# Optimization experiments

Hardware: AMD Instinct MI355X
Metric: run time of the kernel (lower is better)

Reference implementation:

```python
import jax, jax.numpy as jnp
import numpy as np

EMBED = 64
N, T, F = 8, 64, 512

def setup_inputs() -> dict:
    key = jax.random.key(0)
    ks = jax.random.split(key, 8)
    shp = (N, T, F, EMBED)
    s = 1.0 / np.sqrt(EMBED)
    return {
        "value": jax.random.normal(ks[0], shp, jnp.float32),
        "key": jax.random.normal(ks[1], shp, jnp.float32),
        "query": jax.random.normal(ks[2], shp, jnp.float32),
        "Wv": jax.random.normal(ks[3], (EMBED, EMBED), jnp.float32) * s,
        "Wk": jax.random.normal(ks[4], (EMBED, EMBED), jnp.float32) * s,
        "Wq": jax.random.normal(ks[5], (EMBED, EMBED), jnp.float32) * s,
        "Wo": jax.random.normal(ks[6], (EMBED, EMBED), jnp.float32) * s,
        "bo": jax.random.normal(ks[7], (EMBED,), jnp.float32) * 0.01,
    }

def reference(value, key, query, Wv, Wk, Wq, Wo, bo):
    # nn.Linear applies y = x @ W.T (no bias for v/k/q)
    values = jnp.einsum('ntfe,de->ntfd', value, Wv)
    keys = jnp.einsum('ntfe,de->ntfd', key, Wk)
    queries = jnp.einsum('ntfe,de->ntfd', query, Wq)
    # contract over time t; attend over freq (q,k); embed e is a batch dim
    energy = jnp.einsum('ntqe,ntke->neqk', queries, keys)  # [N,e,Fq,Fk]
    scale = jnp.asarray(EMBED, energy.dtype) ** 0.5
    attention = jax.nn.softmax(energy / scale, axis=3)
    out = jnp.einsum('neqk,ntke->ntqe', attention, values)  # [N,T,Fq,e]
    out = jnp.einsum('ntqe,de->ntqd', out, Wo) + bo
    return out
```

## Files before the change

kernel.cpp:

```cpp
#include <hip/hip_runtime.h>
#include <hip/hip_bf16.h>

#define T_ 64
#define F_ 512
#define E_ 64
#define N_ 8
#define PROJ_ELEMS ((size_t)N_ * E_ * F_ * T_)
#define NSLAB ((size_t)E_ * F_ * T_)

typedef short bf16x8 __attribute__((ext_vector_type(8)));
typedef unsigned short u16x8 __attribute__((ext_vector_type(8)));
typedef unsigned short u16x4 __attribute__((ext_vector_type(4)));
typedef float f32x4 __attribute__((ext_vector_type(4)));

static __device__ __forceinline__ f32x4 mfma_bf16(bf16x8 a, bf16x8 b, f32x4 c) {
  return __builtin_amdgcn_mfma_f32_16x16x32_bf16(a, b, c, 0, 0, 0);
}

static __device__ __forceinline__ unsigned short f2bf(float x) {
  union { float f; unsigned u; } v; v.f = x;
  unsigned r = v.u + 0x7fffu + ((v.u >> 16) & 1u);
  return (unsigned short)(r >> 16);
}
static __device__ __forceinline__ float bf2f(unsigned short s) {
  union { unsigned u; float f; } v; v.u = ((unsigned)s) << 16;
  return v.f;
}

static __device__ __forceinline__ unsigned pack_bf16(float lo, float hi) {
#if __has_builtin(__builtin_amdgcn_cvt_pk_bf16_f32)
  typedef __bf16 bf16x2_t __attribute__((ext_vector_type(2)));
  union { bf16x2_t v; unsigned u; } c;
  c.v = __builtin_amdgcn_cvt_pk_bf16_f32(lo, hi);
  return c.u;
#else
  return ((unsigned)f2bf(lo)) | (((unsigned)f2bf(hi)) << 16);
#endif
}

static __device__ __forceinline__ bool detect_f32(const unsigned short* w) {
  bool m = false;
#pragma unroll
  for (int i = 0; i < 64; ++i) m |= ((unsigned)(w[i] & 0x7F80u) >= 0x4000u);
  return m;
}

static __device__ __forceinline__ bf16x8 cvt8(const float* p) {
  float4 x0 = *(const float4*)p;
  float4 x1 = *(const float4*)(p + 4);
  bf16x8 t;
  t[0] = (short)f2bf(x0.x); t[1] = (short)f2bf(x0.y);
  t[2] = (short)f2bf(x0.z); t[3] = (short)f2bf(x0.w);
  t[4] = (short)f2bf(x1.x); t[5] = (short)f2bf(x1.y);
  t[6] = (short)f2bf(x1.z); t[7] = (short)f2bf(x1.w);
  return t;
}

__global__ __launch_bounds__(256) void proj_kernel(
    const void* __restrict__ Xv0, const void* __restrict__ Xv1,
    const void* __restrict__ Xv2, const void* __restrict__ Wv0,
    const void* __restrict__ Wv1, const void* __restrict__ Wv2,
    unsigned short* __restrict__ o0, unsigned short* __restrict__ o1,
    unsigned short* __restrict__ o2, int n_base, int which) {
  __shared__ unsigned short chunk[4 * 64 * 76];
  const int p = (which < 0) ? (int)blockIdx.z : which;
  const void* Xv = (p == 0) ? Xv0 : ((p == 1) ? Xv1 : Xv2);
  const void* Wv = (p == 0) ? Wv0 : ((p == 1) ? Wv1 : Wv2);
  unsigned short* out = (p == 0) ? o0 : ((p == 1) ? o1 : o2);
  const int nb = blockIdx.y;
  const int na = nb + ((p == 2) ? n_base : 0);
  const int f0 = blockIdx.x * 4;
  const int tid = (int)threadIdx.x;
  const int lane = tid & 63, wv = tid >> 6;
  const int lr = lane & 15, quad = lane >> 4;
  const bool f32m = detect_f32((const unsigned short*)Wv);

  bf16x8 wf[4][2];
  if (!f32m) {
    const unsigned short* W = (const unsigned short*)Wv;
#pragma unroll
    for (int dt = 0; dt < 4; ++dt)
#pragma unroll
      for (int h = 0; h < 2; ++h)
        wf[dt][h] = *(const bf16x8*)(W + (dt * 16 + lr) * 64 + h * 32 + quad * 8);
  } else {
    const float* W = (const float*)Wv;
#pragma unroll
    for (int dt = 0; dt < 4; ++dt)
#pragma unroll
      for (int h = 0; h < 2; ++h)
        wf[dt][h] = cvt8(W + (dt * 16 + lr) * 64 + h * 32 + quad * 8);
  }

#pragma unroll
  for (int f = 0; f < 4; ++f) {
    const size_t xoff =
        ((size_t)((na * T_ + wv * 16 + lr) * F_ + f0 + f)) * E_ + quad * 8;
    bf16x8 a0, a1;
    if (!f32m) {
      const unsigned short* xp = (const unsigned short*)Xv + xoff;
      a0 = *(const bf16x8*)xp;
      a1 = *(const bf16x8*)(xp + 32);
    } else {
      const float* xp = (const float*)Xv + xoff;
      a0 = cvt8(xp);
      a1 = cvt8(xp + 32);
    }
#pragma unroll
    for (int dt = 0; dt < 4; ++dt) {
      f32x4 acc = {0.f, 0.f, 0.f, 0.f};
      acc = mfma_bf16(a0, wf[dt][0], acc);
      acc = mfma_bf16(a1, wf[dt][1], acc);
      u16x4 pk;
      pk[0] = f2bf(acc[0]); pk[1] = f2bf(acc[1]);
      pk[2] = f2bf(acc[2]); pk[3] = f2bf(acc[3]);
      *(u16x4*)&chunk[(f * 64 + dt * 16 + lr) * 76 + wv * 16 + quad * 4] = pk;
    }
  }
  __syncthreads();
#pragma unroll
  for (int it = 0; it < 8; ++it) {
    const int slot = it * 256 + tid;
    const int row = slot >> 3;
    const int part = slot & 7;
    const int d = row >> 2;
    const int f = row & 3;
    uint4 v2 = *(const uint4*)&chunk[(f * 64 + d) * 76 + part * 8];
    *(uint4*)(out + ((size_t)((nb * E_ + d) * F_ + f0 + f)) * T_ + part * 8) = v2;
  }
}

__global__ __launch_bounds__(512, 4) void attn_kernel(
    unsigned short* __restrict__ Vp,
    const unsigned short* __restrict__ Kp,
    const unsigned short* __restrict__ Qp, int n_base) {
  __shared__ unsigned short Vlds[T_ * 520];
  __shared__ unsigned short Plds[8 * 16 * 36];
  const int e = blockIdx.x, nb = blockIdx.y;
  const int na = nb + n_base;
  const size_t base = ((size_t)(na * E_ + e)) * (size_t)(F_ * T_);
  const unsigned short* Vb = Vp + base;
  const unsigned short* Kb = Kp + base;
  const unsigned short* Qb = Qp + ((size_t)(nb * E_ + e)) * (size_t)(F_ * T_);
  unsigned short* Ob = Vp + base;
  const int tid = (int)threadIdx.x;

#pragma unroll
  for (int it = 0; it < 8; ++it) {
    int slot = it * 512 + tid;
    int t = slot & 63, kg = slot >> 6;
    u16x8 tv;
#pragma unroll
    for (int j = 0; j < 8; ++j) tv[j] = Vb[(kg * 8 + j) * 64 + t];
    *(u16x8*)&Vlds[t * 520 + kg * 8] = tv;
  }
  __syncthreads();

  const int lane = tid & 63, wv = tid >> 6;
  const int lr = lane & 15, quad = lane >> 4;
  unsigned short* Pl = Plds + wv * (16 * 36);
  const float cexp = 0.18033688011112042f;

#pragma unroll
  for (int iter = 0; iter < 2; ++iter) {
    const int q0 = (wv + iter * 8) * 32;
    bf16x8 qf[2][2];
#pragma unroll
    for (int qt = 0; qt < 2; ++qt) {
      const unsigned short* qp = Qb + (q0 + qt * 16 + lr) * 64 + quad * 8;
      qf[qt][0] = *(const bf16x8*)qp;
      qf[qt][1] = *(const bf16x8*)(qp + 32);
    }
    f32x4 o[2][4];
#pragma unroll
    for (int qt = 0; qt < 2; ++qt)
#pragma unroll
      for (int tt = 0; tt < 4; ++tt) o[qt][tt] = (f32x4){0.f, 0.f, 0.f, 0.f};
    float l0 = 0.f, l1 = 0.f;

    bf16x8 ka[2][2];
#pragma unroll
    for (int h = 0; h < 2; ++h) {
      const unsigned short* kp = Kb + (h * 16 + lr) * 64 + quad * 8;
      ka[h][0] = *(const bf16x8*)kp;
      ka[h][1] = *(const bf16x8*)(kp + 32);
    }

#pragma unroll 1
    for (int kc = 0; kc < 16; ++kc) {
      const int kc1 = (kc + 1) & 15;
      bf16x8 kn[2][2];
#pragma unroll
      for (int h = 0; h < 2; ++h) {
        const unsigned short* kp = Kb + (kc1 * 32 + h * 16 + lr) * 64 + quad * 8;
        kn[h][0] = *(const bf16x8*)kp;
        kn[h][1] = *(const bf16x8*)(kp + 32);
      }
      f32x4 s[2][2];
#pragma unroll
      for (int h = 0; h < 2; ++h)
#pragma unroll
        for (int qt = 0; qt < 2; ++qt) {
          f32x4 acc = {0.f, 0.f, 0.f, 0.f};
          acc = mfma_bf16(ka[h][0], qf[qt][0], acc);
          acc = mfma_bf16(ka[h][1], qf[qt][1], acc);
          s[qt][h] = acc;
        }
      bf16x8 vfr[4];
#pragma unroll
      for (int tt = 0; tt < 4; ++tt)
        vfr[tt] = *(const bf16x8*)&Vlds[(tt * 16 + lr) * 520 + kc * 32 + quad * 8];
#pragma unroll
      for (int qt = 0; qt < 2; ++qt) {
        float lacc = 0.f;
#pragma unroll
        for (int h = 0; h < 2; ++h) {
          float p0 = __builtin_amdgcn_exp2f(s[qt][h][0] * cexp);
          float p1 = __builtin_amdgcn_exp2f(s[qt][h][1] * cexp);
          float p2 = __builtin_amdgcn_exp2f(s[qt][h][2] * cexp);
          float p3 = __builtin_amdgcn_exp2f(s[qt][h][3] * cexp);
          lacc += (p0 + p1) + (p2 + p3);
          uint2 w;
          w.x = pack_bf16(p0, p1);
          w.y = pack_bf16(p2, p3);
          *(uint2*)&Pl[lr * 36 + h * 16 + quad * 4] = w;
        }
        if (qt == 0) l0 += lacc; else l1 += lacc;
        bf16x8 pf = *(const bf16x8*)&Pl[lr * 36 + quad * 8];
#pragma unroll
        for (int tt = 0; tt < 4; ++tt)
          o[qt][tt] = mfma_bf16(vfr[tt], pf, o[qt][tt]);
      }
#pragma unroll
      for (int h = 0; h < 2; ++h) {
        ka[h][0] = kn[h][0];
        ka[h][1] = kn[h][1];
      }
    }
    l0 += __shfl_xor(l0, 16); l0 += __shfl_xor(l0, 32);
    l1 += __shfl_xor(l1, 16); l1 += __shfl_xor(l1, 32);
    const float r0 = __builtin_amdgcn_rcpf(l0);
    const float r1 = __builtin_amdgcn_rcpf(l1);
#pragma unroll
    for (int qt = 0; qt < 2; ++qt) {
      const float rv = qt ? r1 : r0;
#pragma unroll
      for (int tt = 0; tt < 4; ++tt) {
        u16x4 pk;
        pk[0] = f2bf(o[qt][tt][0] * rv);
        pk[1] = f2bf(o[qt][tt][1] * rv);
        pk[2] = f2bf(o[qt][tt][2] * rv);
        pk[3] = f2bf(o[qt][tt][3] * rv);
        *(u16x4*)(Ob + (q0 + qt * 16 + lr) * 64 + tt * 16 + quad * 4) = pk;
      }
    }
  }
}

__global__ __launch_bounds__(256) void outproj_kernel(
    const void* __restrict__ Wov, const void* __restrict__ bov,
    const unsigned short* __restrict__ Obuf, void* __restrict__ outv) {
  const int tid = (int)threadIdx.x;
  const int lane = tid & 63, wv = tid >> 6;
  const int lr = lane & 15, quad = lane >> 4;
  const int unit = (int)blockIdx.x * 4 + wv;
  const int n = unit >> 9, q = unit & 511;
  const bool f32m = detect_f32((const unsigned short*)Wov);

  bf16x8 a[4][2];
  float bias[4][4];
  if (!f32m) {
    const unsigned short* Wo = (const unsigned short*)Wov;
    const unsigned short* bo = (const unsigned short*)bov;
#pragma unroll
    for (int dt = 0; dt < 4; ++dt)
#pragma unroll
      for (int h = 0; h < 2; ++h)
        a[dt][h] = *(const bf16x8*)(Wo + (dt * 16 + lr) * 64 + h * 32 + quad * 8);
#pragma unroll
    for (int dt = 0; dt < 4; ++dt)
#pragma unroll
      for (int r = 0; r < 4; ++r)
        bias[dt][r] = bf2f(bo[dt * 16 + quad * 4 + r]);
  } else {
    const float* Wo = (const float*)Wov;
    const float* bo = (const float*)bov;
#pragma unroll
    for (int dt = 0; dt < 4; ++dt)
#pragma unroll
      for (int h = 0; h < 2; ++h)
        a[dt][h] = cvt8(Wo + (dt * 16 + lr) * 64 + h * 32 + quad * 8);
#pragma unroll
    for (int dt = 0; dt < 4; ++dt)
#pragma unroll
      for (int r = 0; r < 4; ++r)
        bias[dt][r] = bo[dt * 16 + quad * 4 + r];
  }

  const unsigned short* ObBase = Obuf + ((size_t)(n * E_) * F_ + q) * T_;
#pragma unroll
  for (int tt = 0; tt < 4; ++tt) {
    bf16x8 b[2];
#pragma unroll
    for (int h = 0; h < 2; ++h) {
      bf16x8 bv;
#pragma unroll
      for (int j = 0; j < 8; ++j) {
        const int ee = h * 32 + quad * 8 + j;
        bv[j] = (short)ObBase[(size_t)ee * (F_ * T_) + tt * 16 + lr];
      }
      b[h] = bv;
    }
#pragma unroll
    for (int dt = 0; dt < 4; ++dt) {
      f32x4 acc = {0.f, 0.f, 0.f, 0.f};
      acc = mfma_bf16(a[dt][0], b[0], acc);
      acc = mfma_bf16(a[dt][1], b[1], acc);
      const size_t o =
          ((size_t)((n * T_ + tt * 16 + lr) * F_ + q)) * E_ + dt * 16 + quad * 4;
      if (!f32m) {
        u16x4 pk;
        pk[0] = f2bf(acc[0] + bias[dt][0]);
        pk[1] = f2bf(acc[1] + bias[dt][1]);
        pk[2] = f2bf(acc[2] + bias[dt][2]);
        pk[3] = f2bf(acc[3] + bias[dt][3]);
        *(u16x4*)((unsigned short*)outv + o) = pk;
      } else {
        float4 w;
        w.x = acc[0] + bias[dt][0];
        w.y = acc[1] + bias[dt][1];
        w.z = acc[2] + bias[dt][2];
        w.w = acc[3] + bias[dt][3];
        *(float4*)((float*)outv + o) = w;
      }
    }
  }
}

extern "C" void kernel_launch(void* const* d_in, const int* in_sizes, int n_in,
                              void* d_out, int out_size, void* d_ws, size_t ws_size,
                              hipStream_t stream) {
  (void)in_sizes; (void)n_in; (void)out_size;
  const void* value = d_in[0];
  const void* key_  = d_in[1];
  const void* query = d_in[2];
  const void* Wv    = d_in[3];
  const void* Wk    = d_in[4];
  const void* Wq    = d_in[5];
  const void* Wo    = d_in[6];
  const void* bo    = d_in[7];

  unsigned short* Vws  = (unsigned short*)d_ws;
  unsigned short* Qbuf = (unsigned short*)d_ws + PROJ_ELEMS;
  unsigned short* Kbuf = (unsigned short*)d_out;

  long spare = (long)ws_size - (long)(PROJ_ELEMS * 2);
  long qn = spare / (long)(NSLAB * 2);
  int nchunk = qn < 1 ? 1 : (qn > 8 ? 8 : (int)qn);

  if (nchunk >= 8) {
    hipLaunchKernelGGL(proj_kernel, dim3(F_ / 4, N_, 3), dim3(256), 0, stream,
                       value, key_, query, Wv, Wk, Wq, Vws, Kbuf, Qbuf, 0, -1);
    hipLaunchKernelGGL(attn_kernel, dim3(E_, N_), dim3(512), 0, stream,
                       Vws, Kbuf, Qbuf, 0);
  } else {
    hipLaunchKernelGGL(proj_kernel, dim3(F_ / 4, N_, 1), dim3(256), 0, stream,
                       value, key_, query, Wv, Wk, Wq, Vws, Kbuf, Qbuf, 0, 0);
    hipLaunchKernelGGL(proj_kernel, dim3(F_ / 4, N_, 1), dim3(256), 0, stream,
                       value, key_, query, Wv, Wk, Wq, Vws, Kbuf, Qbuf, 0, 1);
    for (int n0 = 0; n0 < N_; n0 += nchunk) {
      int c = (N_ - n0 < nchunk) ? (N_ - n0) : nchunk;
      hipLaunchKernelGGL(proj_kernel, dim3(F_ / 4, c, 1), dim3(256), 0, stream,
                         value, key_, query, Wv, Wk, Wq, Vws, Kbuf, Qbuf, n0, 2);
      hipLaunchKernelGGL(attn_kernel, dim3(E_, c), dim3(512), 0, stream,
                         Vws, Kbuf, Qbuf, n0);
    }
  }
  hipLaunchKernelGGL(outproj_kernel, dim3(1024), dim3(256), 0, stream,
                     Wo, bo, Vws, d_out);
}
```

Measured before the change: 329.0 us.

## Stage attention output through swizzled LDS in outproj and batch proj loads

```diff
diff --git a/kernel.cpp b/kernel.cpp
--- a/kernel.cpp
+++ b/kernel.cpp
@@ -38,6 +38,15 @@
 #endif
 }
 
+static __device__ __forceinline__ bf16x8 cvt2(float4 x0, float4 x1) {
+  union { unsigned u[4]; bf16x8 v; } r;
+  r.u[0] = pack_bf16(x0.x, x0.y);
+  r.u[1] = pack_bf16(x0.z, x0.w);
+  r.u[2] = pack_bf16(x1.x, x1.y);
+  r.u[3] = pack_bf16(x1.z, x1.w);
+  return r.v;
+}
+
 static __device__ __forceinline__ bool detect_f32(const unsigned short* w) {
   bool m = false;
 #pragma unroll
@@ -45,18 +54,7 @@
   return m;
 }
 
-static __device__ __forceinline__ bf16x8 cvt8(const float* p) {
-  float4 x0 = *(const float4*)p;
-  float4 x1 = *(const float4*)(p + 4);
-  bf16x8 t;
-  t[0] = (short)f2bf(x0.x); t[1] = (short)f2bf(x0.y);
-  t[2] = (short)f2bf(x0.z); t[3] = (short)f2bf(x0.w);
-  t[4] = (short)f2bf(x1.x); t[5] = (short)f2bf(x1.y);
-  t[6] = (short)f2bf(x1.z); t[7] = (short)f2bf(x1.w);
-  return t;
-}
-
-__global__ __launch_bounds__(256) void proj_kernel(
+__global__ __launch_bounds__(256, 4) void proj_kernel(
     const void* __restrict__ Xv0, const void* __restrict__ Xv1,
     const void* __restrict__ Xv2, const void* __restrict__ Wv0,
     const void* __restrict__ Wv1, const void* __restrict__ Wv2,
@@ -75,8 +73,16 @@
   const int lr = lane & 15, quad = lane >> 4;
   const bool f32m = detect_f32((const unsigned short*)Wv);
 
+  bf16x8 a0[4], a1[4];
   bf16x8 wf[4][2];
   if (!f32m) {
+#pragma unroll
+    for (int f = 0; f < 4; ++f) {
+      const unsigned short* xp = (const unsigned short*)Xv +
+          ((size_t)((na * T_ + wv * 16 + lr) * F_ + f0 + f)) * E_ + quad * 8;
+      a0[f] = *(const bf16x8*)xp;
+      a1[f] = *(const bf16x8*)(xp + 32);
+    }
     const unsigned short* W = (const unsigned short*)Wv;
 #pragma unroll
     for (int dt = 0; dt < 4; ++dt)
@@ -84,37 +90,42 @@
       for (int h = 0; h < 2; ++h)
         wf[dt][h] = *(const bf16x8*)(W + (dt * 16 + lr) * 64 + h * 32 + quad * 8);
   } else {
+    float4 xr[16];
+#pragma unroll
+    for (int f = 0; f < 4; ++f) {
+      const float* xp = (const float*)Xv +
+          ((size_t)((na * T_ + wv * 16 + lr) * F_ + f0 + f)) * E_ + quad * 8;
+      xr[f * 4 + 0] = *(const float4*)xp;
+      xr[f * 4 + 1] = *(const float4*)(xp + 4);
+      xr[f * 4 + 2] = *(const float4*)(xp + 32);
+      xr[f * 4 + 3] = *(const float4*)(xp + 36);
+    }
     const float* W = (const float*)Wv;
 #pragma unroll
     for (int dt = 0; dt < 4; ++dt)
 #pragma unroll
-      for (int h = 0; h < 2; ++h)
-        wf[dt][h] = cvt8(W + (dt * 16 + lr) * 64 + h * 32 + quad * 8);
+      for (int h = 0; h < 2; ++h) {
+        const float* wp = W + (dt * 16 + lr) * 64 + h * 32 + quad * 8;
+        wf[dt][h] = cvt2(*(const float4*)wp, *(const float4*)(wp + 4));
+      }
+#pragma unroll
+    for (int f = 0; f < 4; ++f) {
+      a0[f] = cvt2(xr[f * 4 + 0], xr[f * 4 + 1]);
+      a1[f] = cvt2(xr[f * 4 + 2], xr[f * 4 + 3]);
+    }
   }
 
 #pragma unroll
   for (int f = 0; f < 4; ++f) {
-    const size_t xoff =
-        ((size_t)((na * T_ + wv * 16 + lr) * F_ + f0 + f)) * E_ + quad * 8;
-    bf16x8 a0, a1;
-    if (!f32m) {
-      const unsigned short* xp = (const unsigned short*)Xv + xoff;
-      a0 = *(const bf16x8*)xp;
-      a1 = *(const bf16x8*)(xp + 32);
-    } else {
-      const float* xp = (const float*)Xv + xoff;
-      a0 = cvt8(xp);
-      a1 = cvt8(xp + 32);
-    }
 #pragma unroll
     for (int dt = 0; dt < 4; ++dt) {
       f32x4 acc = {0.f, 0.f, 0.f, 0.f};
-      acc = mfma_bf16(a0, wf[dt][0], acc);
-      acc = mfma_bf16(a1, wf[dt][1], acc);
-      u16x4 pk;
-      pk[0] = f2bf(acc[0]); pk[1] = f2bf(acc[1]);
-      pk[2] = f2bf(acc[2]); pk[3] = f2bf(acc[3]);
-      *(u16x4*)&chunk[(f * 64 + dt * 16 + lr) * 76 + wv * 16 + quad * 4] = pk;
+      acc = mfma_bf16(a0[f], wf[dt][0], acc);
+      acc = mfma_bf16(a1[f], wf[dt][1], acc);
+      uint2 w;
+      w.x = pack_bf16(acc[0], acc[1]);
+      w.y = pack_bf16(acc[2], acc[3]);
+      *(uint2*)&chunk[(f * 64 + dt * 16 + lr) * 76 + wv * 16 + quad * 4] = w;
     }
   }
   __syncthreads();
@@ -257,15 +268,29 @@
   }
 }
 
-__global__ __launch_bounds__(256) void outproj_kernel(
+__global__ __launch_bounds__(256, 4) void outproj_kernel(
     const void* __restrict__ Wov, const void* __restrict__ bov,
     const unsigned short* __restrict__ Obuf, void* __restrict__ outv) {
+  __shared__ unsigned short Olds[256 * 64];
   const int tid = (int)threadIdx.x;
   const int lane = tid & 63, wv = tid >> 6;
   const int lr = lane & 15, quad = lane >> 4;
-  const int unit = (int)blockIdx.x * 4 + wv;
-  const int n = unit >> 9, q = unit & 511;
+  const int blk = (int)blockIdx.x;
+  const int n = blk >> 7;
+  const int q0 = (blk & 127) * 4;
   const bool f32m = detect_f32((const unsigned short*)Wov);
+
+  const unsigned short* Ob0 = Obuf + ((size_t)(n * E_) * F_ + q0) * T_;
+#pragma unroll
+  for (int it = 0; it < 8; ++it) {
+    const int slot = it * 256 + tid;
+    const int row = slot >> 3;
+    const int part = slot & 7;
+    const int e = row >> 2, q = row & 3;
+    const int ps = part ^ (((row >> 5) & 3) << 1);
+    uint4 v = *(const uint4*)(Ob0 + ((size_t)e * F_ + q) * T_ + part * 8);
+    *(uint4*)&Olds[row * 64 + ps * 8] = v;
+  }
 
   bf16x8 a[4][2];
   float bias[4][4];
@@ -288,16 +313,19 @@
 #pragma unroll
     for (int dt = 0; dt < 4; ++dt)
 #pragma unroll
-      for (int h = 0; h < 2; ++h)
-        a[dt][h] = cvt8(Wo + (dt * 16 + lr) * 64 + h * 32 + quad * 8);
+      for (int h = 0; h < 2; ++h) {
+        const float* wp = Wo + (dt * 16 + lr) * 64 + h * 32 + quad * 8;
+        a[dt][h] = cvt2(*(const float4*)wp, *(const float4*)(wp + 4));
+      }
 #pragma unroll
     for (int dt = 0; dt < 4; ++dt)
 #pragma unroll
       for (int r = 0; r < 4; ++r)
         bias[dt][r] = bo[dt * 16 + quad * 4 + r];
   }
-
-  const unsigned short* ObBase = Obuf + ((size_t)(n * E_) * F_ + q) * T_;
+  __syncthreads();
+
+  const int q = q0 + wv;
 #pragma unroll
   for (int tt = 0; tt < 4; ++tt) {
     bf16x8 b[2];
@@ -307,7 +335,9 @@
 #pragma unroll
       for (int j = 0; j < 8; ++j) {
         const int ee = h * 32 + quad * 8 + j;
-        bv[j] = (short)ObBase[(size_t)ee * (F_ * T_) + tt * 16 + lr];
+        const int row = ee * 4 + wv;
+        const int cc = (tt * 2 + (lr >> 3)) ^ (((ee >> 3) & 3) << 1);
+        bv[j] = (short)Olds[row * 64 + cc * 8 + (lr & 7)];
       }
       b[h] = bv;
     }
```

Measured after the change: 326.7 us. Within noise of the previous version (-0.7%).
